# Performance work log

Hardware: AMD Instinct MI355X
Metric: run time of the kernel (lower is better)

## Reference

```python
import jax, jax.numpy as jnp
import numpy as np

T, B, D_IN, D_H = 1024, 128, 256, 256


def setup_inputs() -> dict:
    key = jax.random.key(0)
    ks = jax.random.split(key, 9)
    s_in = 1.0 / np.sqrt(D_IN + D_H)  # torch nn.Linear init scale
    inputs = jax.random.normal(ks[0], (T, B, D_IN), dtype=jnp.float32)
    def lin(kw, kb):
        W = jax.random.uniform(kw, (D_IN + D_H, D_H), jnp.float32, -s_in, s_in)
        b = jax.random.uniform(kb, (D_H,), jnp.float32, -s_in, s_in)
        return W, b
    Wf, bf = lin(ks[1], ks[2])
    Wi, bi = lin(ks[3], ks[4])
    Wg, bg = lin(ks[5], ks[6])
    Wo, bo = lin(ks[7], ks[8])
    return {"inputs": inputs, "Wf": Wf, "bf": bf, "Wi": Wi, "bi": bi,
            "Wg": Wg, "bg": bg, "Wo": Wo, "bo": bo}


def reference(inputs, Wf, bf, Wi, bi, Wg, bg, Wo, bo):
    Bsz = inputs.shape[1]
    h0 = jnp.zeros((Bsz, D_H), inputs.dtype)
    c0 = jnp.zeros((Bsz, D_H), inputs.dtype)

    def step(carry, x):
        hx, cx = carry
        combined = jnp.concatenate([x, hx], axis=1)  # [B, D_IN+D_H]
        f = jax.nn.sigmoid(combined @ Wf + bf)
        i = jax.nn.sigmoid(combined @ Wi + bi)
        g = jnp.tanh(combined @ Wg + bg)
        o = jax.nn.sigmoid(combined @ Wo + bo)
        cx = f * cx + i * g
        hx = o * jnp.tanh(cx)
        return (hx, cx), hx

    (hx, cx), outputs = jax.lax.scan(step, (h0, c0), inputs)
    return outputs, (hx, cx)
```

## Files before the change

kernel.cpp:

```cpp
#include <hip/hip_runtime.h>
#include <hip/hip_bf16.h>

typedef short s16x8 __attribute__((ext_vector_type(8)));
typedef int   i32x4 __attribute__((ext_vector_type(4)));
typedef float f32x4 __attribute__((ext_vector_type(4)));
typedef float f32x2 __attribute__((ext_vector_type(2)));

#define T_STEPS 1024
#define BATCH   128
#define DIN     256
#define DH      256
#define NWG     64
#define NTHREADS 256

static __device__ __forceinline__ short f2bf(float f){ return __builtin_bit_cast(short,(__bf16)f); }
static __device__ __forceinline__ float sigf(float x){ return 1.f/(1.f+__expf(-x)); }
static __device__ __forceinline__ float tanhfast(float x){ return 1.f-2.f/(1.f+__expf(2.f*x)); }

static __device__ __forceinline__ i32x4 ld16_cc(const void* p){
  i32x4 r; asm volatile("global_load_dwordx4 %0, %1, off sc0 sc1" : "=v"(r) : "v"(p) : "memory"); return r;
}
static __device__ __forceinline__ unsigned ld4_cc(const void* p){
  unsigned r; asm volatile("global_load_dword %0, %1, off sc0 sc1\ns_waitcnt vmcnt(0)" : "=v"(r) : "v"(p) : "memory"); return r;
}
static __device__ __forceinline__ void st4_cc(void* p, unsigned v){
  asm volatile("global_store_dword %0, %1, off sc0 sc1" :: "v"(p), "v"(v) : "memory");
}
static __device__ __forceinline__ void st8_p(void* p, f32x2 v){
  asm volatile("global_store_dwordx2 %0, %1, off" :: "v"(p), "v"(v) : "memory");
}

static __device__ __forceinline__ s16x8 cvt8(f32x4 a, f32x4 b){
  s16x8 r;
  r[0]=f2bf(a[0]); r[1]=f2bf(a[1]); r[2]=f2bf(a[2]); r[3]=f2bf(a[3]);
  r[4]=f2bf(b[0]); r[5]=f2bf(b[1]); r[6]=f2bf(b[2]); r[7]=f2bf(b[3]);
  return r;
}

__global__ __launch_bounds__(NTHREADS, 1)
void lstm_v10(const float* __restrict__ X,
              const float* __restrict__ Wf, const float* __restrict__ bfv,
              const float* __restrict__ Wi, const float* __restrict__ biv,
              const float* __restrict__ Wg, const float* __restrict__ bgv,
              const float* __restrict__ Wo, const float* __restrict__ bov,
              float* __restrict__ out,
              unsigned short* __restrict__ hbuf,
              unsigned int* __restrict__ flags,
              int needEnd)
{
  const int bid = blockIdx.x;
  const int g   = bid & 7;
  const int csl = bid >> 3;
  const int tid = threadIdx.x;
  const int lane = tid & 63, wv = tid >> 6;
  const int grp = lane >> 4, l15 = lane & 15;
  const int r0 = g * 16;

  __shared__ short bfx_unused[4];
  __shared__ short a_lds[2 * 32 * 16 * 8];
  __shared__ float elds[4 * 16 * 36];
  (void)bfx_unused;

  s16x8 bfr[2][16];
  {
    const float* Wm[4] = {Wf, Wi, Wg, Wo};
    const int gate = l15 >> 2, jj = l15 & 3;
    const float* Wsrc = Wm[gate];
#pragma unroll
    for (int n2 = 0; n2 < 2; ++n2) {
      const int hc = csl * 32 + (wv * 2 + n2) * 4 + jj;
#pragma unroll
      for (int kk = 0; kk < 16; ++kk) {
        const float* p = Wsrc + (size_t)(kk * 32 + grp * 8) * DH + hc;
        s16x8 f;
#pragma unroll
        for (int s = 0; s < 8; ++s) f[s] = f2bf(p[(size_t)s * DH]);
        bfr[n2][kk] = f;
      }
    }
  }

  const int colg = csl * 32 + wv * 8 + 2 * grp;
  float bia[4][2];
  {
    const float* Bv[4] = {bfv, biv, bgv, bov};
#pragma unroll
    for (int q = 0; q < 4; ++q) { bia[q][0] = Bv[q][colg]; bia[q][1] = Bv[q][colg + 1]; }
  }

  const int xrow = tid & 15, xseg = tid >> 4;

  f32x4 xp0, xp1, xp2, xp3;
  {
    const float* xs = X + (size_t)(r0 + xrow) * DIN + xseg * 16;
    s16x8 lo = cvt8(*(const f32x4*)xs, *(const f32x4*)(xs + 4));
    s16x8 hi = cvt8(*(const f32x4*)(xs + 8), *(const f32x4*)(xs + 12));
    *(s16x8*)&a_lds[((2 * xseg + 0) * 16 + xrow) * 8] = lo;
    *(s16x8*)&a_lds[((2 * xseg + 1) * 16 + xrow) * 8] = hi;
    const float* xn = X + ((size_t)1 * BATCH + r0 + xrow) * DIN + xseg * 16;
    xp0 = *(const f32x4*)xn;       xp1 = *(const f32x4*)(xn + 4);
    xp2 = *(const f32x4*)(xn + 8); xp3 = *(const f32x4*)(xn + 12);
  }
  __syncthreads();

  unsigned* myflag = flags + (g * 32 + csl * 4 + wv);
  const unsigned* pollp = flags + (g * 32 + (lane & 31));
  float* eldsw = &elds[wv * 16 * 36];
  float cs0 = 0.f, cs1 = 0.f, h0s = 0.f, h1s = 0.f;

  for (int t = 0; t < T_STEPS; ++t) {
    while (1) {
      unsigned v = ld4_cc(pollp);
      if (__all((int)(v >= (unsigned)t))) break;
    }
    __builtin_amdgcn_sched_barrier(0);

    const unsigned short* hr = hbuf + (size_t)(t & 1) * (BATCH * DH)
                             + (size_t)(r0 + l15) * DH + grp * 8;
    i32x4 hraw[8];
#pragma unroll
    for (int q = 0; q < 8; ++q) hraw[q] = ld16_cc(hr + q * 32);

    {
      short* ab = a_lds + ((t + 1) & 1) * (32 * 16 * 8);
      s16x8 lo = cvt8(xp0, xp1), hi = cvt8(xp2, xp3);
      *(s16x8*)&ab[((2 * xseg + 0) * 16 + xrow) * 8] = lo;
      *(s16x8*)&ab[((2 * xseg + 1) * 16 + xrow) * 8] = hi;
    }

    const short* ar = a_lds + (t & 1) * (32 * 16 * 8);
    f32x4 acc0 = {0.f,0.f,0.f,0.f}, acc1 = {0.f,0.f,0.f,0.f};
#pragma unroll
    for (int kk = 0; kk < 8; ++kk) {
      s16x8 a = *(const s16x8*)&ar[((kk * 4 + grp) * 16 + l15) * 8];
      acc0 = __builtin_amdgcn_mfma_f32_16x16x32_bf16(a, bfr[0][kk], acc0, 0, 0, 0);
      acc1 = __builtin_amdgcn_mfma_f32_16x16x32_bf16(a, bfr[1][kk], acc1, 0, 0, 0);
    }

    asm volatile("s_waitcnt vmcnt(0)" ::: "memory");
    __builtin_amdgcn_sched_barrier(0);
#pragma unroll
    for (int q = 0; q < 8; ++q) {
      s16x8 ah = __builtin_bit_cast(s16x8, hraw[q]);
      acc0 = __builtin_amdgcn_mfma_f32_16x16x32_bf16(ah, bfr[0][8 + q], acc0, 0, 0, 0);
      acc1 = __builtin_amdgcn_mfma_f32_16x16x32_bf16(ah, bfr[1][8 + q], acc1, 0, 0, 0);
    }

#pragma unroll
    for (int rr = 0; rr < 4; ++rr) {
      eldsw[(grp * 4 + rr) * 36 + l15]      = acc0[rr];
      eldsw[(grp * 4 + rr) * 36 + 16 + l15] = acc1[rr];
    }
    asm volatile("s_waitcnt lgkmcnt(0)" ::: "memory");
    __builtin_amdgcn_sched_barrier(0);
    float z0[4], z1[4];
    const int hc0 = 2 * grp, hc1 = 2 * grp + 1;
#pragma unroll
    for (int q = 0; q < 4; ++q) {
      z0[q] = eldsw[l15 * 36 + ((hc0 >> 2) << 4) + 4 * q + (hc0 & 3)];
      z1[q] = eldsw[l15 * 36 + ((hc1 >> 2) << 4) + 4 * q + (hc1 & 3)];
    }
    {
      float zf = z0[0] + bia[0][0], zi = z0[1] + bia[1][0];
      float zg = z0[2] + bia[2][0], zo = z0[3] + bia[3][0];
      cs0 = sigf(zf) * cs0 + sigf(zi) * tanhfast(zg);
      h0s = sigf(zo) * tanhfast(cs0);
    }
    {
      float zf = z1[0] + bia[0][1], zi = z1[1] + bia[1][1];
      float zg = z1[2] + bia[2][1], zo = z1[3] + bia[3][1];
      cs1 = sigf(zf) * cs1 + sigf(zi) * tanhfast(zg);
      h1s = sigf(zo) * tanhfast(cs1);
    }

    const int row = r0 + l15;
    {
      unsigned hpk = (unsigned)(unsigned short)f2bf(h0s)
                   | ((unsigned)(unsigned short)f2bf(h1s) << 16);
      st4_cc(hbuf + (size_t)((t + 1) & 1) * (BATCH * DH)
             + (size_t)row * DH + colg, hpk);
      f32x2 ov; ov[0] = h0s; ov[1] = h1s;
      st8_p(out + ((size_t)t * BATCH + row) * DH + colg, ov);
    }

    asm volatile("s_waitcnt vmcnt(1)" ::: "memory");
    if (lane == 0) st4_cc(myflag, (unsigned)(t + 1));

    {
      const int tp = (t + 2 < T_STEPS) ? t + 2 : T_STEPS - 1;
      const float* xs = X + ((size_t)tp * BATCH + r0 + xrow) * DIN + xseg * 16;
      xp0 = *(const f32x4*)xs;       xp1 = *(const f32x4*)(xs + 4);
      xp2 = *(const f32x4*)(xs + 8); xp3 = *(const f32x4*)(xs + 12);
    }
  }

  if (needEnd) {
    const unsigned* fp = flags + tid;
    while (ld4_cc(fp) < (unsigned)T_STEPS) __builtin_amdgcn_s_sleep(1);
    __syncthreads();
  }
  {
    const size_t base = (size_t)T_STEPS * BATCH * DH;
    const size_t idx  = (size_t)(r0 + l15) * DH + colg;
    out[base + idx]     = h0s;
    out[base + idx + 1] = h1s;
    out[base + BATCH * DH + idx]     = cs0;
    out[base + BATCH * DH + idx + 1] = cs1;
  }
}

extern "C" void kernel_launch(void* const* d_in, const int* in_sizes, int n_in,
                              void* d_out, int out_size, void* d_ws, size_t ws_size,
                              hipStream_t stream) {
  const float* X   = (const float*)d_in[0];
  const float* Wf  = (const float*)d_in[1];
  const float* bf_ = (const float*)d_in[2];
  const float* Wi  = (const float*)d_in[3];
  const float* bi_ = (const float*)d_in[4];
  const float* Wg  = (const float*)d_in[5];
  const float* bg_ = (const float*)d_in[6];
  const float* Wo  = (const float*)d_in[7];
  const float* bo_ = (const float*)d_in[8];
  float* out = (float*)d_out;

  const size_t hbytes = (size_t)2 * BATCH * DH * 2;
  const size_t fbytes = 1024;
  unsigned short* hbuf;
  unsigned int*   flags;
  int needEnd;
  if (ws_size >= hbytes + fbytes) {
    hbuf  = (unsigned short*)d_ws;
    flags = (unsigned int*)((unsigned char*)d_ws + hbytes);
    needEnd = 0;
    hipMemsetAsync(d_ws, 0, hbytes + fbytes, stream);
  } else {
    unsigned char* tail = (unsigned char*)d_out + (size_t)T_STEPS * BATCH * DH * 4;
    hbuf  = (unsigned short*)tail;
    flags = (unsigned int*)(tail + hbytes);
    needEnd = 1;
    hipMemsetAsync(tail, 0, hbytes + fbytes, stream);
  }

  lstm_v10<<<NWG, NTHREADS, 0, stream>>>(X, Wf, bf_, Wi, bi_, Wg, bg_,
                                         Wo, bo_, out, hbuf, flags, needEnd);
}
```

Before: 4.302 ms.

## Tag hidden-state words with timestep to validate data and reduce flag traffic

The new kernel stores each bf16 hidden value in a 32-bit word whose upper half holds the timestep. Consumers check these tags after loading and reload until every tag matches, instead of depending only on per-wave flags. Flags are now one per workgroup, written after an intra-block barrier, so pollers read 8 flags instead of 32. The epilogue is reorganised through a wider LDS tile so each thread owns contiguous output columns and writes them with an 8-byte store. In exchange, hidden-state traffic doubles, a second block barrier is added per step, and the old kernel is kept as a fallback when the workspace is too small.

```diff
diff --git a/kernel.cpp b/kernel.cpp
--- a/kernel.cpp
+++ b/kernel.cpp
@@ -3,6 +3,7 @@
 
 typedef short s16x8 __attribute__((ext_vector_type(8)));
 typedef int   i32x4 __attribute__((ext_vector_type(4)));
+typedef unsigned u32x2 __attribute__((ext_vector_type(2)));
 typedef float f32x4 __attribute__((ext_vector_type(4)));
 typedef float f32x2 __attribute__((ext_vector_type(2)));
 
@@ -26,6 +27,9 @@
 static __device__ __forceinline__ void st4_cc(void* p, unsigned v){
   asm volatile("global_store_dword %0, %1, off sc0 sc1" :: "v"(p), "v"(v) : "memory");
 }
+static __device__ __forceinline__ void st8t_cc(void* p, u32x2 v){
+  asm volatile("global_store_dwordx2 %0, %1, off sc0 sc1" :: "v"(p), "v"(v) : "memory");
+}
 static __device__ __forceinline__ void st8_p(void* p, f32x2 v){
   asm volatile("global_store_dwordx2 %0, %1, off" :: "v"(p), "v"(v) : "memory");
 }
@@ -38,15 +42,14 @@
 }
 
 __global__ __launch_bounds__(NTHREADS, 1)
-void lstm_v10(const float* __restrict__ X,
+void lstm_v11(const float* __restrict__ X,
               const float* __restrict__ Wf, const float* __restrict__ bfv,
               const float* __restrict__ Wi, const float* __restrict__ biv,
               const float* __restrict__ Wg, const float* __restrict__ bgv,
               const float* __restrict__ Wo, const float* __restrict__ bov,
               float* __restrict__ out,
-              unsigned short* __restrict__ hbuf,
-              unsigned int* __restrict__ flags,
-              int needEnd)
+              unsigned* __restrict__ htag,
+              unsigned* __restrict__ flags)
 {
   const int bid = blockIdx.x;
   const int g   = bid & 7;
@@ -56,10 +59,8 @@
   const int grp = lane >> 4, l15 = lane & 15;
   const int r0 = g * 16;
 
-  __shared__ short bfx_unused[4];
   __shared__ short a_lds[2 * 32 * 16 * 8];
-  __shared__ float elds[4 * 16 * 36];
-  (void)bfx_unused;
+  __shared__ float elds[16 * 132];
 
   s16x8 bfr[2][16];
   {
@@ -80,16 +81,21 @@
     }
   }
 
-  const int colg = csl * 32 + wv * 8 + 2 * grp;
+  const int erow = tid >> 4;
+  const int j2   = tid & 15;
+  const int ntl  = j2 >> 1;
+  const int jjl  = (j2 & 1) * 2;
   float bia[4][2];
   {
     const float* Bv[4] = {bfv, biv, bgv, bov};
 #pragma unroll
-    for (int q = 0; q < 4; ++q) { bia[q][0] = Bv[q][colg]; bia[q][1] = Bv[q][colg + 1]; }
+    for (int q = 0; q < 4; ++q) {
+      bia[q][0] = Bv[q][csl * 32 + 2 * j2];
+      bia[q][1] = Bv[q][csl * 32 + 2 * j2 + 1];
+    }
   }
 
   const int xrow = tid & 15, xseg = tid >> 4;
-
   f32x4 xp0, xp1, xp2, xp3;
   {
     const float* xs = X + (size_t)(r0 + xrow) * DIN + xseg * 16;
@@ -103,6 +109,200 @@
   }
   __syncthreads();
 
+  unsigned* myflag = flags + (g * 32 + csl);
+  const unsigned* pollp = flags + (g * 32 + (lane & 7));
+  float cs0 = 0.f, cs1 = 0.f, h0s = 0.f, h1s = 0.f;
+
+  for (int t = 0; t < T_STEPS; ++t) {
+    const unsigned tte = (unsigned)t << 16;
+
+    while (1) {
+      unsigned v = ld4_cc(pollp);
+      if (__all((int)(v >= (unsigned)t))) break;
+    }
+    __builtin_amdgcn_sched_barrier(0);
+
+    const unsigned* hb = htag + (size_t)(t & 1) * (BATCH * DH)
+                       + (size_t)(r0 + l15) * DH + grp * 8;
+    i32x4 hraw[16];
+#pragma unroll
+    for (int q = 0; q < 8; ++q) {
+      hraw[2 * q]     = ld16_cc(hb + q * 32);
+      hraw[2 * q + 1] = ld16_cc(hb + q * 32 + 4);
+    }
+
+    {
+      short* ab = a_lds + ((t + 1) & 1) * (32 * 16 * 8);
+      s16x8 lo = cvt8(xp0, xp1), hi = cvt8(xp2, xp3);
+      *(s16x8*)&ab[((2 * xseg + 0) * 16 + xrow) * 8] = lo;
+      *(s16x8*)&ab[((2 * xseg + 1) * 16 + xrow) * 8] = hi;
+    }
+
+    const short* ar = a_lds + (t & 1) * (32 * 16 * 8);
+    f32x4 acc0 = {0.f,0.f,0.f,0.f}, acc1 = {0.f,0.f,0.f,0.f};
+#pragma unroll
+    for (int kk = 0; kk < 8; ++kk) {
+      s16x8 a = *(const s16x8*)&ar[((kk * 4 + grp) * 16 + l15) * 8];
+      acc0 = __builtin_amdgcn_mfma_f32_16x16x32_bf16(a, bfr[0][kk], acc0, 0, 0, 0);
+      acc1 = __builtin_amdgcn_mfma_f32_16x16x32_bf16(a, bfr[1][kk], acc1, 0, 0, 0);
+    }
+
+    asm volatile("s_waitcnt vmcnt(0)" ::: "memory");
+    __builtin_amdgcn_sched_barrier(0);
+    {
+      int guardo = 1 << 16;
+      while (1) {
+        unsigned bad = 0;
+#pragma unroll
+        for (int i = 0; i < 16; ++i)
+          bad |= (unsigned)(hraw[i][0] ^ (int)tte) | (unsigned)(hraw[i][1] ^ (int)tte)
+               | (unsigned)(hraw[i][2] ^ (int)tte) | (unsigned)(hraw[i][3] ^ (int)tte);
+        bad &= 0xFFFF0000u;
+        if (__all((int)(bad == 0))) break;
+        if (--guardo < 0) break;
+#pragma unroll
+        for (int q = 0; q < 8; ++q) {
+          hraw[2 * q]     = ld16_cc(hb + q * 32);
+          hraw[2 * q + 1] = ld16_cc(hb + q * 32 + 4);
+        }
+        asm volatile("s_waitcnt vmcnt(0)" ::: "memory");
+        __builtin_amdgcn_sched_barrier(0);
+      }
+    }
+
+#pragma unroll
+    for (int q = 0; q < 8; ++q) {
+      i32x4 hp;
+      hp[0] = (int)__builtin_amdgcn_perm((unsigned)hraw[2*q][1],   (unsigned)hraw[2*q][0],   0x05040100u);
+      hp[1] = (int)__builtin_amdgcn_perm((unsigned)hraw[2*q][3],   (unsigned)hraw[2*q][2],   0x05040100u);
+      hp[2] = (int)__builtin_amdgcn_perm((unsigned)hraw[2*q+1][1], (unsigned)hraw[2*q+1][0], 0x05040100u);
+      hp[3] = (int)__builtin_amdgcn_perm((unsigned)hraw[2*q+1][3], (unsigned)hraw[2*q+1][2], 0x05040100u);
+      s16x8 ah = __builtin_bit_cast(s16x8, hp);
+      acc0 = __builtin_amdgcn_mfma_f32_16x16x32_bf16(ah, bfr[0][8 + q], acc0, 0, 0, 0);
+      acc1 = __builtin_amdgcn_mfma_f32_16x16x32_bf16(ah, bfr[1][8 + q], acc1, 0, 0, 0);
+    }
+
+#pragma unroll
+    for (int rr = 0; rr < 4; ++rr) {
+      elds[(grp * 4 + rr) * 132 + (wv * 2 + 0) * 16 + l15] = acc0[rr];
+      elds[(grp * 4 + rr) * 132 + (wv * 2 + 1) * 16 + l15] = acc1[rr];
+    }
+    asm volatile("s_waitcnt lgkmcnt(0)" ::: "memory");
+    __builtin_amdgcn_sched_barrier(0);
+    __builtin_amdgcn_s_barrier();
+    __builtin_amdgcn_sched_barrier(0);
+
+    const float* ez = &elds[erow * 132 + ntl * 16];
+    float h0, h1;
+    {
+      float zf = ez[0 + jjl] + bia[0][0], zi = ez[4 + jjl] + bia[1][0];
+      float zg = ez[8 + jjl] + bia[2][0], zo = ez[12 + jjl] + bia[3][0];
+      float cn = sigf(zf) * cs0 + sigf(zi) * tanhfast(zg);
+      h0 = sigf(zo) * tanhfast(cn); cs0 = cn; h0s = h0;
+    }
+    {
+      float zf = ez[1 + jjl] + bia[0][1], zi = ez[5 + jjl] + bia[1][1];
+      float zg = ez[9 + jjl] + bia[2][1], zo = ez[13 + jjl] + bia[3][1];
+      float cn = sigf(zf) * cs1 + sigf(zi) * tanhfast(zg);
+      h1 = sigf(zo) * tanhfast(cn); cs1 = cn; h1s = h1;
+    }
+
+    const int rowg = r0 + erow;
+    {
+      const unsigned ttw = (unsigned)(t + 1) << 16;
+      u32x2 hp2;
+      hp2[0] = (unsigned)(unsigned short)f2bf(h0) | ttw;
+      hp2[1] = (unsigned)(unsigned short)f2bf(h1) | ttw;
+      st8t_cc(htag + (size_t)((t + 1) & 1) * (BATCH * DH)
+              + (size_t)rowg * DH + csl * 32 + 2 * j2, hp2);
+    }
+    __builtin_amdgcn_sched_barrier(0);
+    __builtin_amdgcn_s_barrier();
+    __builtin_amdgcn_sched_barrier(0);
+    if (tid == 0) st4_cc(myflag, (unsigned)(t + 1));
+
+    {
+      f32x2 ov; ov[0] = h0; ov[1] = h1;
+      st8_p(out + ((size_t)t * BATCH + rowg) * DH + csl * 32 + 2 * j2, ov);
+    }
+    {
+      const int tp = (t + 2 < T_STEPS) ? t + 2 : T_STEPS - 1;
+      const float* xs = X + ((size_t)tp * BATCH + r0 + xrow) * DIN + xseg * 16;
+      xp0 = *(const f32x4*)xs;       xp1 = *(const f32x4*)(xs + 4);
+      xp2 = *(const f32x4*)(xs + 8); xp3 = *(const f32x4*)(xs + 12);
+    }
+  }
+
+  {
+    const size_t base = (size_t)T_STEPS * BATCH * DH;
+    const size_t idx  = (size_t)(r0 + erow) * DH + csl * 32 + 2 * j2;
+    out[base + idx]     = h0s;
+    out[base + idx + 1] = h1s;
+    out[base + BATCH * DH + idx]     = cs0;
+    out[base + BATCH * DH + idx + 1] = cs1;
+  }
+}
+
+__global__ __launch_bounds__(NTHREADS, 1)
+void lstm_v10_fb(const float* __restrict__ X,
+                 const float* __restrict__ Wf, const float* __restrict__ bfv,
+                 const float* __restrict__ Wi, const float* __restrict__ biv,
+                 const float* __restrict__ Wg, const float* __restrict__ bgv,
+                 const float* __restrict__ Wo, const float* __restrict__ bov,
+                 float* __restrict__ out,
+                 unsigned short* __restrict__ hbuf,
+                 unsigned int* __restrict__ flags)
+{
+  const int bid = blockIdx.x;
+  const int g   = bid & 7;
+  const int csl = bid >> 3;
+  const int tid = threadIdx.x;
+  const int lane = tid & 63, wv = tid >> 6;
+  const int grp = lane >> 4, l15 = lane & 15;
+  const int r0 = g * 16;
+
+  __shared__ short a_lds[2 * 32 * 16 * 8];
+  __shared__ float elds[4 * 16 * 36];
+
+  s16x8 bfr[2][16];
+  {
+    const float* Wm[4] = {Wf, Wi, Wg, Wo};
+    const int gate = l15 >> 2, jj = l15 & 3;
+    const float* Wsrc = Wm[gate];
+#pragma unroll
+    for (int n2 = 0; n2 < 2; ++n2) {
+      const int hc = csl * 32 + (wv * 2 + n2) * 4 + jj;
+#pragma unroll
+      for (int kk = 0; kk < 16; ++kk) {
+        const float* p = Wsrc + (size_t)(kk * 32 + grp * 8) * DH + hc;
+        s16x8 f;
+#pragma unroll
+        for (int s = 0; s < 8; ++s) f[s] = f2bf(p[(size_t)s * DH]);
+        bfr[n2][kk] = f;
+      }
+    }
+  }
+  const int colg = csl * 32 + wv * 8 + 2 * grp;
+  float bia[4][2];
+  {
+    const float* Bv[4] = {bfv, biv, bgv, bov};
+#pragma unroll
+    for (int q = 0; q < 4; ++q) { bia[q][0] = Bv[q][colg]; bia[q][1] = Bv[q][colg + 1]; }
+  }
+  const int xrow = tid & 15, xseg = tid >> 4;
+  f32x4 xp0, xp1, xp2, xp3;
+  {
+    const float* xs = X + (size_t)(r0 + xrow) * DIN + xseg * 16;
+    s16x8 lo = cvt8(*(const f32x4*)xs, *(const f32x4*)(xs + 4));
+    s16x8 hi = cvt8(*(const f32x4*)(xs + 8), *(const f32x4*)(xs + 12));
+    *(s16x8*)&a_lds[((2 * xseg + 0) * 16 + xrow) * 8] = lo;
+    *(s16x8*)&a_lds[((2 * xseg + 1) * 16 + xrow) * 8] = hi;
+    const float* xn = X + ((size_t)1 * BATCH + r0 + xrow) * DIN + xseg * 16;
+    xp0 = *(const f32x4*)xn;       xp1 = *(const f32x4*)(xn + 4);
+    xp2 = *(const f32x4*)(xn + 8); xp3 = *(const f32x4*)(xn + 12);
+  }
+  __syncthreads();
+
   unsigned* myflag = flags + (g * 32 + csl * 4 + wv);
   const unsigned* pollp = flags + (g * 32 + (lane & 31));
   float* eldsw = &elds[wv * 16 * 36];
@@ -114,20 +314,17 @@
       if (__all((int)(v >= (unsigned)t))) break;
     }
     __builtin_amdgcn_sched_barrier(0);
-
     const unsigned short* hr = hbuf + (size_t)(t & 1) * (BATCH * DH)
                              + (size_t)(r0 + l15) * DH + grp * 8;
     i32x4 hraw[8];
 #pragma unroll
     for (int q = 0; q < 8; ++q) hraw[q] = ld16_cc(hr + q * 32);
-
     {
       short* ab = a_lds + ((t + 1) & 1) * (32 * 16 * 8);
       s16x8 lo = cvt8(xp0, xp1), hi = cvt8(xp2, xp3);
       *(s16x8*)&ab[((2 * xseg + 0) * 16 + xrow) * 8] = lo;
       *(s16x8*)&ab[((2 * xseg + 1) * 16 + xrow) * 8] = hi;
     }
-
     const short* ar = a_lds + (t & 1) * (32 * 16 * 8);
     f32x4 acc0 = {0.f,0.f,0.f,0.f}, acc1 = {0.f,0.f,0.f,0.f};
 #pragma unroll
@@ -136,7 +333,6 @@
       acc0 = __builtin_amdgcn_mfma_f32_16x16x32_bf16(a, bfr[0][kk], acc0, 0, 0, 0);
       acc1 = __builtin_amdgcn_mfma_f32_16x16x32_bf16(a, bfr[1][kk], acc1, 0, 0, 0);
     }
-
     asm volatile("s_waitcnt vmcnt(0)" ::: "memory");
     __builtin_amdgcn_sched_barrier(0);
 #pragma unroll
@@ -145,7 +341,6 @@
       acc0 = __builtin_amdgcn_mfma_f32_16x16x32_bf16(ah, bfr[0][8 + q], acc0, 0, 0, 0);
       acc1 = __builtin_amdgcn_mfma_f32_16x16x32_bf16(ah, bfr[1][8 + q], acc1, 0, 0, 0);
     }
-
 #pragma unroll
     for (int rr = 0; rr < 4; ++rr) {
       eldsw[(grp * 4 + rr) * 36 + l15]      = acc0[rr];
@@ -172,7 +367,6 @@
       cs1 = sigf(zf) * cs1 + sigf(zi) * tanhfast(zg);
       h1s = sigf(zo) * tanhfast(cs1);
     }
-
     const int row = r0 + l15;
     {
       unsigned hpk = (unsigned)(unsigned short)f2bf(h0s)
@@ -182,10 +376,8 @@
       f32x2 ov; ov[0] = h0s; ov[1] = h1s;
       st8_p(out + ((size_t)t * BATCH + row) * DH + colg, ov);
     }
-
     asm volatile("s_waitcnt vmcnt(1)" ::: "memory");
     if (lane == 0) st4_cc(myflag, (unsigned)(t + 1));
-
     {
       const int tp = (t + 2 < T_STEPS) ? t + 2 : T_STEPS - 1;
       const float* xs = X + ((size_t)tp * BATCH + r0 + xrow) * DIN + xseg * 16;
@@ -193,8 +385,7 @@
       xp2 = *(const f32x4*)(xs + 8); xp3 = *(const f32x4*)(xs + 12);
     }
   }
-
-  if (needEnd) {
+  {
     const unsigned* fp = flags + tid;
     while (ld4_cc(fp) < (unsigned)T_STEPS) __builtin_amdgcn_s_sleep(1);
     __syncthreads();
@@ -223,24 +414,20 @@
   const float* bo_ = (const float*)d_in[8];
   float* out = (float*)d_out;
 
-  const size_t hbytes = (size_t)2 * BATCH * DH * 2;
-  const size_t fbytes = 1024;
-  unsigned short* hbuf;
-  unsigned int*   flags;
-  int needEnd;
-  if (ws_size >= hbytes + fbytes) {
-    hbuf  = (unsigned short*)d_ws;
-    flags = (unsigned int*)((unsigned char*)d_ws + hbytes);
-    needEnd = 0;
-    hipMemsetAsync(d_ws, 0, hbytes + fbytes, stream);
-  } else {
-    unsigned char* tail = (unsigned char*)d_out + (size_t)T_STEPS * BATCH * DH * 4;
-    hbuf  = (unsigned short*)tail;
-    flags = (unsigned int*)(tail + hbytes);
-    needEnd = 1;
-    hipMemsetAsync(tail, 0, hbytes + fbytes, stream);
-  }
-
-  lstm_v10<<<NWG, NTHREADS, 0, stream>>>(X, Wf, bf_, Wi, bi_, Wg, bg_,
-                                         Wo, bo_, out, hbuf, flags, needEnd);
-}
+  const size_t tagbytes = (size_t)2 * BATCH * DH * 4;
+  const size_t fbytes   = 1024;
+  if (ws_size >= tagbytes + fbytes) {
+    unsigned* htag  = (unsigned*)d_ws;
+    unsigned* flags = (unsigned*)((unsigned char*)d_ws + tagbytes);
+    hipMemsetAsync(d_ws, 0, tagbytes + fbytes, stream);
+    lstm_v11<<<NWG, NTHREADS, 0, stream>>>(X, Wf, bf_, Wi, bi_, Wg, bg_,
+                                           Wo, bo_, out, htag, flags);
+    return;
+  }
+  unsigned char* tail = (unsigned char*)d_out + (size_t)T_STEPS * BATCH * DH * 4;
+  unsigned short* hbuf = (unsigned short*)tail;
+  unsigned int* flags  = (unsigned int*)(tail + 131072);
+  hipMemsetAsync(tail, 0, 131072 + 1024, stream);
+  lstm_v10_fb<<<NWG, NTHREADS, 0, stream>>>(X, Wf, bf_, Wi, bi_, Wg, bg_,
+                                            Wo, bo_, out, hbuf, flags);
+}
```

New measurement: 3.761 ms. 1.14x faster.
